# Performance work log

Measured on AMD Instinct MI355X. Metric: run time of the kernel, lower is better.

Reference implementation:

```python
import jax, jax.numpy as jnp
import numpy as np

N_A, N_C, N_L = 50000, 10000, 10000
HID = 128


def _gatv2(x_src, x_dst, src, dst, ea, Wl, bl, Wr, br, We, att, bias, H):
    # GATv2Conv (PyG) bipartite, edge_dim=1, concat=False (mean over heads), eval mode (no dropout)
    C = bias.shape[0]
    n_dst = x_dst.shape[0]
    xl = (x_src @ Wl + bl).reshape(-1, H, C)      # [N_src, H, C]
    xr = (x_dst @ Wr + br).reshape(-1, H, C)      # [N_dst, H, C]
    e = jax.nn.leaky_relu(xl[src] + xr[dst] + (ea @ We).reshape(-1, H, C), 0.2)  # [E,H,C]
    logit = jnp.einsum('ehc,hc->eh', e, att)      # [E,H]
    m = jax.ops.segment_max(logit, dst, num_segments=n_dst)
    m = jax.lax.stop_gradient(jnp.where(jnp.isfinite(m), m, 0.0))
    ex = jnp.exp(logit - m[dst])
    denom = jax.ops.segment_sum(ex, dst, num_segments=n_dst)
    alpha = ex / (denom[dst] + 1e-16)             # segment softmax over incoming edges
    out = jax.ops.segment_sum(alpha[:, :, None] * xl[src], dst, num_segments=n_dst)
    return out.mean(axis=1) + bias                # concat=False -> head mean + bias


def setup_inputs() -> dict:
    key = jax.random.key(0)
    ks = iter(jax.random.split(key, 80))
    def rn(shape, s=1.0):
        return jax.random.normal(next(ks), shape, jnp.float32) * s
    inp = {}
    inp['x_asset'] = rn((N_A, 512))
    inp['x_creator'] = rn((N_C, 2))
    inp['x_licensee'] = rn((N_L, 1))
    # edges: (name, E, src_max, dst_max)
    edges = [('cb', 50000, N_A, N_C), ('lt', 100000, N_A, N_L), ('sim', 200000, N_A, N_A),
             ('fw', 100000, N_A, N_A), ('rcb', 50000, N_C, N_A), ('rlt', 100000, N_L, N_A)]
    for name, E, smax, dmax in edges:
        inp[f'{name}_src'] = jax.random.randint(next(ks), (E,), 0, smax, jnp.int32)
        inp[f'{name}_dst'] = jax.random.randint(next(ks), (E,), 0, dmax, jnp.int32)
        inp[f'ea_{name}'] = rn((E, 1))
    w = 0.05  # param scale
    inp['Wp_a'] = rn((512, HID), w); inp['bp_a'] = rn((HID,), w)
    inp['Wp_c'] = rn((2, HID), w);   inp['bp_c'] = rn((HID,), w)
    inp['Wp_l'] = rn((1, HID), w);   inp['bp_l'] = rn((HID,), w)
    # layer 1: heads=2, stacked over the 6 relations
    H1 = 2
    inp['Wl1'] = rn((6, HID, H1 * HID), w); inp['bl1'] = rn((6, H1 * HID), w)
    inp['Wr1'] = rn((6, HID, H1 * HID), w); inp['br1'] = rn((6, H1 * HID), w)
    inp['We1'] = rn((6, 1, H1 * HID), w)
    inp['att1'] = rn((6, H1, HID), w); inp['bias1'] = rn((6, HID), w)
    # layer 2: heads=1
    inp['Wl2'] = rn((6, HID, HID), w); inp['bl2'] = rn((6, HID), w)
    inp['Wr2'] = rn((6, HID, HID), w); inp['br2'] = rn((6, HID), w)
    inp['We2'] = rn((6, 1, HID), w)
    inp['att2'] = rn((6, 1, HID), w); inp['bias2'] = rn((6, HID), w)
    inp['Wc1'] = rn((HID, HID), w); inp['bc1'] = rn((HID,), w)
    inp['Wc2'] = rn((HID, 3), w);   inp['bc2'] = rn((3,), w)
    inp['query_asset_index'] = 123
    return inp


def reference(x_asset, x_creator, x_licensee, Wp_a, bp_a, Wp_c, bp_c, Wp_l, bp_l,
              Wl1, bl1, Wr1, br1, We1, att1, bias1,
              Wl2, bl2, Wr2, br2, We2, att2, bias2,
              Wc1, bc1, Wc2, bc2,
              ea_cb, ea_lt, ea_sim, ea_fw, ea_rcb, ea_rlt,
              cb_src, cb_dst, lt_src, lt_dst, sim_src, sim_dst,
              fw_src, fw_dst, rcb_src, rcb_dst, rlt_src, rlt_dst,
              query_asset_index):
    x = {'Asset': x_asset @ Wp_a + bp_a,
         'Creator': x_creator @ Wp_c + bp_c,
         'Licensee': x_licensee @ Wp_l + bp_l}
    rels = [('Asset', 'Creator', cb_src, cb_dst, ea_cb),
            ('Asset', 'Licensee', lt_src, lt_dst, ea_lt),
            ('Asset', 'Asset', sim_src, sim_dst, ea_sim),
            ('Asset', 'Asset', fw_src, fw_dst, ea_fw),
            ('Creator', 'Asset', rcb_src, rcb_dst, ea_rcb),
            ('Licensee', 'Asset', rlt_src, rlt_dst, ea_rlt)]

    def hetero_layer(x, Wl, bl, Wr, br, We, att, bias, H):
        out = {k: jnp.zeros((v.shape[0], HID), v.dtype) for k, v in x.items()}
        for i, (st, dt, s, d, ea) in enumerate(rels):  # HeteroConv aggr='sum'
            out[dt] = out[dt] + _gatv2(x[st], x[dt], s, d, ea,
                                       Wl[i], bl[i], Wr[i], br[i], We[i], att[i], bias[i], H)
        return out

    x = hetero_layer(x, Wl1, bl1, Wr1, br1, We1, att1, bias1, 2)
    x = {k: jax.nn.relu(v) for k, v in x.items()}  # eval: dropout is identity
    x = hetero_layer(x, Wl2, bl2, Wr2, br2, We2, att2, bias2, 1)
    x = {k: jax.nn.relu(v) for k, v in x.items()}
    a = x['Asset'][query_asset_index]
    return jax.nn.relu(a @ Wc1 + bc1) @ Wc2 + bc2
```

## Files before the change

kernel.cpp:

```cpp
#include <hip/hip_runtime.h>
#include <math.h>

#define FAMAX 512
#define FCMAX 256
#define FLMAX 256
#define N1MAX 4096
#define N2MAX 512

struct Inputs {
  const float *x_asset, *x_creator, *x_licensee;
  const float *Wp_a,*bp_a,*Wp_c,*bp_c,*Wp_l,*bp_l;
  const float *Wl1,*bl1,*Wr1,*br1,*We1,*att1,*bias1;
  const float *Wl2,*bl2,*Wr2,*br2,*We2,*att2,*bias2;
  const float *Wc1,*bc1,*Wc2,*bc2;
};

struct Edges {
  const int *cb_s,*cb_d;  const float* ea_cb;  int Ecb;
  const int *lt_s,*lt_d;  const float* ea_lt;  int Elt;
  const int *sim_s,*sim_d;const float* ea_sim; int Esim;
  const int *fw_s,*fw_d;  const float* ea_fw;  int Efw;
  const int *rcb_s,*rcb_d;const float* ea_rcb; int Ercb;
  const int *rlt_s,*rlt_d;const float* ea_rlt; int Erlt;
};

struct WSP {
  int* cnt;
  int* flagA; int* flagC; int* flagL;
  int* fa; int* fc; int* fl;
  int* l2rel; int* l2src; float* l2ea;
  int* l1rel; int* l1src; int* l1dslot; float* l1ea;
  float* xr1a;
  float* xr1c;
  float* xr1l;
  float* xl1e;
  float* logit1;
  float* x1a;
  float* x1c;
  float* x1l;
  float* xr2q;
  float* xl2e;
  float* logit2;
};

__device__ __forceinline__ float leaky(float x){ return x > 0.f ? x : 0.2f*x; }

__device__ void proj_node(int type, int node, const Inputs& in, float* h0){
  int t = threadIdx.x;
  if (t < 128) {
    float acc;
    if (type == 0) {
      acc = in.bp_a[t];
      const float* xr = in.x_asset + (long long)node*512;
      for (int k=0;k<512;k++) acc = fmaf(xr[k], in.Wp_a[k*128+t], acc);
    } else if (type == 1) {
      acc = in.bp_c[t] + in.x_creator[node*2]*in.Wp_c[t] + in.x_creator[node*2+1]*in.Wp_c[128+t];
    } else {
      acc = in.bp_l[t] + in.x_licensee[node]*in.Wp_l[t];
    }
    h0[t] = acc;
  }
  __syncthreads();
}

__global__ void k1_scan_l2(Edges eg, const int* qptr, WSP w){
  int q = qptr[0];
  if (blockIdx.x==0 && threadIdx.x==0) w.flagA[q] = 1;
  int total = eg.Esim + eg.Efw + eg.Ercb + eg.Erlt;
  for (int i = blockIdx.x*blockDim.x + threadIdx.x; i < total; i += gridDim.x*blockDim.x){
    int j = i, rel; const int *sp,*dp; const float* ep;
    if (j < eg.Esim){ rel=2; sp=eg.sim_s; dp=eg.sim_d; ep=eg.ea_sim; }
    else { j -= eg.Esim;
      if (j < eg.Efw){ rel=3; sp=eg.fw_s; dp=eg.fw_d; ep=eg.ea_fw; }
      else { j -= eg.Efw;
        if (j < eg.Ercb){ rel=4; sp=eg.rcb_s; dp=eg.rcb_d; ep=eg.ea_rcb; }
        else { j -= eg.Ercb; rel=5; sp=eg.rlt_s; dp=eg.rlt_d; ep=eg.ea_rlt; }
      }
    }
    if (dp[j] == q){
      int src = sp[j];
      int k = atomicAdd(&w.cnt[0], 1);
      if (k < N2MAX){ w.l2rel[k]=rel; w.l2src[k]=src; w.l2ea[k]=ep[j]; }
      if (rel <= 3) w.flagA[src] = 1;
      else if (rel == 4) w.flagC[src] = 1;
      else w.flagL[src] = 1;
    }
  }
}

__global__ void k2_compact(WSP w){
  int i = blockIdx.x*blockDim.x + threadIdx.x;
  if (i < 50000){
    if (w.flagA[i] == 1){ int k = atomicAdd(&w.cnt[1],1);
      if (k < FAMAX){ w.flagA[i]=k+2; w.fa[k]=i; } else w.flagA[i]=0; }
  } else if (i < 60000){ int n=i-50000;
    if (w.flagC[n] == 1){ int k = atomicAdd(&w.cnt[2],1);
      if (k < FCMAX){ w.flagC[n]=k+2; w.fc[k]=n; } else w.flagC[n]=0; }
  } else if (i < 70000){ int n=i-60000;
    if (w.flagL[n] == 1){ int k = atomicAdd(&w.cnt[3],1);
      if (k < FLMAX){ w.flagL[n]=k+2; w.fl[k]=n; } else w.flagL[n]=0; }
  }
}

__global__ void k3_scan_l1(Edges eg, WSP w){
  int total = eg.Ecb+eg.Elt+eg.Esim+eg.Efw+eg.Ercb+eg.Erlt;
  for (int i = blockIdx.x*blockDim.x + threadIdx.x; i < total; i += gridDim.x*blockDim.x){
    int j = i, rel; const int *sp,*dp; const float* ep; const int* flag;
    if (j < eg.Ecb){ rel=0; sp=eg.cb_s; dp=eg.cb_d; ep=eg.ea_cb; flag=w.flagC; }
    else { j -= eg.Ecb;
    if (j < eg.Elt){ rel=1; sp=eg.lt_s; dp=eg.lt_d; ep=eg.ea_lt; flag=w.flagL; }
    else { j -= eg.Elt;
    if (j < eg.Esim){ rel=2; sp=eg.sim_s; dp=eg.sim_d; ep=eg.ea_sim; flag=w.flagA; }
    else { j -= eg.Esim;
    if (j < eg.Efw){ rel=3; sp=eg.fw_s; dp=eg.fw_d; ep=eg.ea_fw; flag=w.flagA; }
    else { j -= eg.Efw;
    if (j < eg.Ercb){ rel=4; sp=eg.rcb_s; dp=eg.rcb_d; ep=eg.ea_rcb; flag=w.flagA; }
    else { j -= eg.Ercb; rel=5; sp=eg.rlt_s; dp=eg.rlt_d; ep=eg.ea_rlt; flag=w.flagA; }}}}}
    int f = flag[dp[j]];
    if (f >= 2){
      int k = atomicAdd(&w.cnt[4], 1);
      if (k < N1MAX){ w.l1rel[k]=rel; w.l1src[k]=sp[j]; w.l1dslot[k]=f-2; w.l1ea[k]=ep[j]; }
    }
  }
}

__global__ void k4_xr1(Inputs in, WSP w){
  __shared__ float h0[128];
  int b = blockIdx.x;
  int na = w.cnt[1] < FAMAX ? w.cnt[1] : FAMAX;
  int nc = w.cnt[2] < FCMAX ? w.cnt[2] : FCMAX;
  int nl = w.cnt[3] < FLMAX ? w.cnt[3] : FLMAX;
  int rel; float* dst;
  if (b < FAMAX*4){
    int slot = b>>2, ridx = b&3;
    if (slot >= na) return;
    rel = 2 + ridx;
    proj_node(0, w.fa[slot], in, h0);
    dst = w.xr1a + ((size_t)slot*4 + ridx)*256;
  } else if (b < FAMAX*4 + FCMAX){
    int slot = b - FAMAX*4;
    if (slot >= nc) return;
    rel = 0;
    proj_node(1, w.fc[slot], in, h0);
    dst = w.xr1c + (size_t)slot*256;
  } else {
    int slot = b - FAMAX*4 - FCMAX;
    if (slot >= nl) return;
    rel = 1;
    proj_node(2, w.fl[slot], in, h0);
    dst = w.xr1l + (size_t)slot*256;
  }
  int j = threadIdx.x;
  float acc = in.br1[rel*256 + j];
  const float* W = in.Wr1 + (size_t)rel*128*256;
  for (int c=0;c<128;c++) acc = fmaf(h0[c], W[c*256 + j], acc);
  dst[j] = acc;
}

__global__ void k5_l1edge(Inputs in, WSP w){
  __shared__ float h0[128];
  __shared__ float red[256];
  int i = blockIdx.x;
  int n = w.cnt[4] < N1MAX ? w.cnt[4] : N1MAX;
  if (i >= n) return;
  int rel = w.l1rel[i], src = w.l1src[i], dslot = w.l1dslot[i];
  float ea = w.l1ea[i];
  int stype = (rel <= 3) ? 0 : (rel == 4 ? 1 : 2);
  proj_node(stype, src, in, h0);
  int j = threadIdx.x;
  float acc = in.bl1[rel*256 + j];
  const float* W = in.Wl1 + (size_t)rel*128*256;
  for (int c=0;c<128;c++) acc = fmaf(h0[c], W[c*256 + j], acc);
  w.xl1e[(size_t)i*256 + j] = acc;
  const float* xr;
  if (rel >= 2) xr = w.xr1a + ((size_t)dslot*4 + (rel-2))*256;
  else if (rel == 0) xr = w.xr1c + (size_t)dslot*256;
  else xr = w.xr1l + (size_t)dslot*256;
  float e = leaky(acc + xr[j] + ea*in.We1[rel*256 + j]);
  int h = j >> 7, c = j & 127;
  red[j] = e * in.att1[(rel*2 + h)*128 + c];
  __syncthreads();
  for (int s=64; s>0; s>>=1){ if (c < s) red[j] += red[j+s]; __syncthreads(); }
  if (c == 0) w.logit1[i*2 + h] = red[j];
}

__global__ void k6_agg(Inputs in, WSP w){
  int b = blockIdx.x;
  int na = w.cnt[1] < FAMAX ? w.cnt[1] : FAMAX;
  int nc = w.cnt[2] < FCMAX ? w.cnt[2] : FCMAX;
  int nl = w.cnt[3] < FLMAX ? w.cnt[3] : FLMAX;
  int type, slot;
  if (b < FAMAX){ slot = b; if (slot >= na) return; type = 0; }
  else if (b < FAMAX+FCMAX){ slot = b-FAMAX; if (slot >= nc) return; type = 1; }
  else { slot = b-FAMAX-FCMAX; if (slot >= nl) return; type = 2; }
  int n1 = w.cnt[4] < N1MAX ? w.cnt[4] : N1MAX;
  int j = threadIdx.x;
  float out = 0.f;
  int r0, r1;
  if (type == 0){ r0=2; r1=5; } else if (type == 1){ r0=0; r1=0; } else { r0=1; r1=1; }
  for (int r=r0; r<=r1; r++){
    out += in.bias1[r*128 + j];
    float m0 = -INFINITY, m1 = -INFINITY;
    for (int i=0;i<n1;i++){
      if (w.l1rel[i]==r && w.l1dslot[i]==slot){
        m0 = fmaxf(m0, w.logit1[i*2]);
        m1 = fmaxf(m1, w.logit1[i*2+1]);
      }
    }
    if (m0 == -INFINITY) continue;
    float d0=0.f, d1=0.f, a0=0.f, a1=0.f;
    for (int i=0;i<n1;i++){
      if (w.l1rel[i]==r && w.l1dslot[i]==slot){
        float e0 = expf(w.logit1[i*2]   - m0);
        float e1 = expf(w.logit1[i*2+1] - m1);
        d0 += e0; d1 += e1;
        a0 = fmaf(e0, w.xl1e[(size_t)i*256 + j], a0);
        a1 = fmaf(e1, w.xl1e[(size_t)i*256 + 128 + j], a1);
      }
    }
    out += 0.5f*(a0/(d0+1e-16f) + a1/(d1+1e-16f));
  }
  float v = fmaxf(out, 0.f);
  if (type == 0) w.x1a[slot*128 + j] = v;
  else if (type == 1) w.x1c[slot*128 + j] = v;
  else w.x1l[slot*128 + j] = v;
}

__global__ void k7_xr2(Inputs in, WSP w, const int* qptr){
  int q = qptr[0];
  int qslot = w.flagA[q] - 2;
  const float* xq = w.x1a + (size_t)qslot*128;
  int j = threadIdx.x;
  for (int ridx=0; ridx<4; ridx++){
    int r = 2 + ridx;
    float acc = in.br2[r*128 + j];
    const float* W = in.Wr2 + (size_t)r*128*128;
    for (int c=0;c<128;c++) acc = fmaf(xq[c], W[c*128 + j], acc);
    w.xr2q[ridx*128 + j] = acc;
  }
}

__global__ void k8_l2edge(Inputs in, WSP w){
  __shared__ float red[128];
  int i = blockIdx.x;
  int n2 = w.cnt[0] < N2MAX ? w.cnt[0] : N2MAX;
  if (i >= n2) return;
  int rel = w.l2rel[i], src = w.l2src[i];
  float ea = w.l2ea[i];
  int f;
  const float* xbase;
  if (rel <= 3){ f = w.flagA[src]; xbase = w.x1a; }
  else if (rel == 4){ f = w.flagC[src]; xbase = w.x1c; }
  else { f = w.flagL[src]; xbase = w.x1l; }
  if (f < 2) return;
  const float* xsrc = xbase + (size_t)(f-2)*128;
  int j = threadIdx.x;
  float acc = in.bl2[rel*128 + j];
  const float* W = in.Wl2 + (size_t)rel*128*128;
  for (int c=0;c<128;c++) acc = fmaf(xsrc[c], W[c*128 + j], acc);
  w.xl2e[(size_t)i*128 + j] = acc;
  float e = leaky(acc + w.xr2q[(rel-2)*128 + j] + ea*in.We2[rel*128 + j]);
  red[j] = e * in.att2[rel*128 + j];
  __syncthreads();
  for (int s=64; s>0; s>>=1){ if (j < s) red[j] += red[j+s]; __syncthreads(); }
  if (j == 0) w.logit2[i] = red[0];
}

__global__ void k9_final(Inputs in, WSP w, float* out){
  __shared__ float x2[128];
  __shared__ float t[128];
  int n2 = w.cnt[0] < N2MAX ? w.cnt[0] : N2MAX;
  int j = threadIdx.x;
  float o = 0.f;
  for (int r=2; r<=5; r++){
    o += in.bias2[r*128 + j];
    float m = -INFINITY;
    for (int i=0;i<n2;i++) if (w.l2rel[i]==r) m = fmaxf(m, w.logit2[i]);
    if (m == -INFINITY) continue;
    float d = 0.f, acc = 0.f;
    for (int i=0;i<n2;i++) if (w.l2rel[i]==r){
      float e = expf(w.logit2[i] - m);
      d += e;
      acc = fmaf(e, w.xl2e[(size_t)i*128 + j], acc);
    }
    o += acc/(d + 1e-16f);
  }
  x2[j] = fmaxf(o, 0.f);
  __syncthreads();
  float acc = in.bc1[j];
  for (int c=0;c<128;c++) acc = fmaf(x2[c], in.Wc1[c*128 + j], acc);
  t[j] = fmaxf(acc, 0.f);
  __syncthreads();
  if (j < 3){
    float r = in.bc2[j];
    for (int c=0;c<128;c++) r = fmaf(t[c], in.Wc2[c*3 + j], r);
    out[j] = r;
  }
}

extern "C" void kernel_launch(void* const* d_in, const int* in_sizes, int n_in,
                              void* d_out, int out_size, void* d_ws, size_t ws_size,
                              hipStream_t stream){
  Inputs in;
  in.x_asset   = (const float*)d_in[0];
  in.x_creator = (const float*)d_in[1];
  in.x_licensee= (const float*)d_in[2];
  Edges eg;
  eg.cb_s =(const int*)d_in[3];  eg.cb_d =(const int*)d_in[4];  eg.ea_cb =(const float*)d_in[5];  eg.Ecb = in_sizes[3];
  eg.lt_s =(const int*)d_in[6];  eg.lt_d =(const int*)d_in[7];  eg.ea_lt =(const float*)d_in[8];  eg.Elt = in_sizes[6];
  eg.sim_s=(const int*)d_in[9];  eg.sim_d=(const int*)d_in[10]; eg.ea_sim=(const float*)d_in[11]; eg.Esim= in_sizes[9];
  eg.fw_s =(const int*)d_in[12]; eg.fw_d =(const int*)d_in[13]; eg.ea_fw =(const float*)d_in[14]; eg.Efw = in_sizes[12];
  eg.rcb_s=(const int*)d_in[15]; eg.rcb_d=(const int*)d_in[16]; eg.ea_rcb=(const float*)d_in[17]; eg.Ercb= in_sizes[15];
  eg.rlt_s=(const int*)d_in[18]; eg.rlt_d=(const int*)d_in[19]; eg.ea_rlt=(const float*)d_in[20]; eg.Erlt= in_sizes[18];
  in.Wp_a=(const float*)d_in[21]; in.bp_a=(const float*)d_in[22];
  in.Wp_c=(const float*)d_in[23]; in.bp_c=(const float*)d_in[24];
  in.Wp_l=(const float*)d_in[25]; in.bp_l=(const float*)d_in[26];
  in.Wl1=(const float*)d_in[27]; in.bl1=(const float*)d_in[28];
  in.Wr1=(const float*)d_in[29]; in.br1=(const float*)d_in[30];
  in.We1=(const float*)d_in[31]; in.att1=(const float*)d_in[32]; in.bias1=(const float*)d_in[33];
  in.Wl2=(const float*)d_in[34]; in.bl2=(const float*)d_in[35];
  in.Wr2=(const float*)d_in[36]; in.br2=(const float*)d_in[37];
  in.We2=(const float*)d_in[38]; in.att2=(const float*)d_in[39]; in.bias2=(const float*)d_in[40];
  in.Wc1=(const float*)d_in[41]; in.bc1=(const float*)d_in[42];
  in.Wc2=(const float*)d_in[43]; in.bc2=(const float*)d_in[44];
  const int* qptr = (const int*)d_in[45];

  char* p = (char*)d_ws;
  auto carve = [&](size_t n)->char*{ char* r = p; p += ((n + 255) & ~(size_t)255); return r; };
  WSP w;
  w.cnt    = (int*)carve(16*4);
  w.flagA  = (int*)carve(50000*4);
  w.flagC  = (int*)carve(10000*4);
  w.flagL  = (int*)carve(10000*4);
  size_t zero_bytes = (size_t)(p - (char*)d_ws);
  w.fa = (int*)carve(FAMAX*4); w.fc = (int*)carve(FCMAX*4); w.fl = (int*)carve(FLMAX*4);
  w.l2rel=(int*)carve(N2MAX*4); w.l2src=(int*)carve(N2MAX*4); w.l2ea=(float*)carve(N2MAX*4);
  w.l1rel=(int*)carve(N1MAX*4); w.l1src=(int*)carve(N1MAX*4); w.l1dslot=(int*)carve(N1MAX*4); w.l1ea=(float*)carve(N1MAX*4);
  w.xr1a=(float*)carve((size_t)FAMAX*4*256*4);
  w.xr1c=(float*)carve((size_t)FCMAX*256*4);
  w.xr1l=(float*)carve((size_t)FLMAX*256*4);
  w.xl1e=(float*)carve((size_t)N1MAX*256*4);
  w.logit1=(float*)carve((size_t)N1MAX*2*4);
  w.x1a=(float*)carve((size_t)FAMAX*128*4);
  w.x1c=(float*)carve((size_t)FCMAX*128*4);
  w.x1l=(float*)carve((size_t)FLMAX*128*4);
  w.xr2q=(float*)carve(4*128*4);
  w.xl2e=(float*)carve((size_t)N2MAX*128*4);
  w.logit2=(float*)carve(N2MAX*4);

  hipMemsetAsync(d_ws, 0, zero_bytes, stream);

  int tE2 = eg.Esim + eg.Efw + eg.Ercb + eg.Erlt;
  k1_scan_l2<<<(tE2+255)/256, 256, 0, stream>>>(eg, qptr, w);
  k2_compact<<<(70000+255)/256, 256, 0, stream>>>(w);
  int tE1 = eg.Ecb + eg.Elt + tE2;
  k3_scan_l1<<<(tE1+255)/256, 256, 0, stream>>>(eg, w);
  k4_xr1<<<FAMAX*4 + FCMAX + FLMAX, 256, 0, stream>>>(in, w);
  k5_l1edge<<<N1MAX, 256, 0, stream>>>(in, w);
  k6_agg<<<FAMAX + FCMAX + FLMAX, 128, 0, stream>>>(in, w);
  k7_xr2<<<1, 128, 0, stream>>>(in, w, qptr);
  k8_l2edge<<<N2MAX, 128, 0, stream>>>(in, w);
  k9_final<<<1, 128, 0, stream>>>(in, w, (float*)d_out);
}
```

Measured before the change: 346.8 us.

## Fuse GNN pipeline into five kernels with atomic claim and shrunk capacity caps

Replaces the separate flag-compaction pass with an atomicCAS-based claim done inside the layer-2 edge scan. The xr projection, edge logits and softmax aggregation are fused into a per-node kernel, and the layer-2 xr/edge/final stages are merged into one single-block kernel. Capacity caps (FAMAX, N1MAX, N2MAX and others) are cut sharply, and new DMAX/N2C limits are added. This removes four launches and several large workspace buffers, but node-side work is serialised per edge with block syncs, and the smaller caps can silently drop neighbours if real degrees exceed them.

After: 359.9 us. 1.04x slower.

```diff
diff --git a/kernel.cpp b/kernel.cpp
--- a/kernel.cpp
+++ b/kernel.cpp
@@ -1,11 +1,13 @@
 #include <hip/hip_runtime.h>
 #include <math.h>
 
-#define FAMAX 512
-#define FCMAX 256
-#define FLMAX 256
-#define N1MAX 4096
-#define N2MAX 512
+#define FAMAX 64
+#define FCMAX 32
+#define FLMAX 32
+#define N1MAX 1024
+#define N2MAX 128
+#define DMAX  64
+#define N2C   64
 
 struct Inputs {
   const float *x_asset, *x_creator, *x_licensee;
@@ -30,20 +32,22 @@
   int* fa; int* fc; int* fl;
   int* l2rel; int* l2src; float* l2ea;
   int* l1rel; int* l1src; int* l1dslot; float* l1ea;
-  float* xr1a;
-  float* xr1c;
-  float* xr1l;
   float* xl1e;
-  float* logit1;
   float* x1a;
   float* x1c;
   float* x1l;
-  float* xr2q;
-  float* xl2e;
-  float* logit2;
 };
 
 __device__ __forceinline__ float leaky(float x){ return x > 0.f ? x : 0.2f*x; }
+
+__device__ __forceinline__ void claim(int* flag, int* cnt, int* list, int node, int cap){
+  int old = atomicCAS(&flag[node], 0, 1);
+  if (old == 0){
+    int k = atomicAdd(cnt, 1);
+    if (k < cap){ list[k] = node; atomicExch(&flag[node], k + 2); }
+    else atomicExch(&flag[node], 0);
+  }
+}
 
 __device__ void proj_node(int type, int node, const Inputs& in, float* h0){
   int t = threadIdx.x;
@@ -65,7 +69,7 @@
 
 __global__ void k1_scan_l2(Edges eg, const int* qptr, WSP w){
   int q = qptr[0];
-  if (blockIdx.x==0 && threadIdx.x==0) w.flagA[q] = 1;
+  if (blockIdx.x==0 && threadIdx.x==0) claim(w.flagA, &w.cnt[1], w.fa, q, FAMAX);
   int total = eg.Esim + eg.Efw + eg.Ercb + eg.Erlt;
   for (int i = blockIdx.x*blockDim.x + threadIdx.x; i < total; i += gridDim.x*blockDim.x){
     int j = i, rel; const int *sp,*dp; const float* ep;
@@ -81,28 +85,14 @@
       int src = sp[j];
       int k = atomicAdd(&w.cnt[0], 1);
       if (k < N2MAX){ w.l2rel[k]=rel; w.l2src[k]=src; w.l2ea[k]=ep[j]; }
-      if (rel <= 3) w.flagA[src] = 1;
-      else if (rel == 4) w.flagC[src] = 1;
-      else w.flagL[src] = 1;
-    }
-  }
-}
-
-__global__ void k2_compact(WSP w){
-  int i = blockIdx.x*blockDim.x + threadIdx.x;
-  if (i < 50000){
-    if (w.flagA[i] == 1){ int k = atomicAdd(&w.cnt[1],1);
-      if (k < FAMAX){ w.flagA[i]=k+2; w.fa[k]=i; } else w.flagA[i]=0; }
-  } else if (i < 60000){ int n=i-50000;
-    if (w.flagC[n] == 1){ int k = atomicAdd(&w.cnt[2],1);
-      if (k < FCMAX){ w.flagC[n]=k+2; w.fc[k]=n; } else w.flagC[n]=0; }
-  } else if (i < 70000){ int n=i-60000;
-    if (w.flagL[n] == 1){ int k = atomicAdd(&w.cnt[3],1);
-      if (k < FLMAX){ w.flagL[n]=k+2; w.fl[k]=n; } else w.flagL[n]=0; }
-  }
-}
-
-__global__ void k3_scan_l1(Edges eg, WSP w){
+      if (rel <= 3) claim(w.flagA, &w.cnt[1], w.fa, src, FAMAX);
+      else if (rel == 4) claim(w.flagC, &w.cnt[2], w.fc, src, FCMAX);
+      else claim(w.flagL, &w.cnt[3], w.fl, src, FLMAX);
+    }
+  }
+}
+
+__global__ void k2_scan_l1(Edges eg, WSP w){
   int total = eg.Ecb+eg.Elt+eg.Esim+eg.Efw+eg.Ercb+eg.Erlt;
   for (int i = blockIdx.x*blockDim.x + threadIdx.x; i < total; i += gridDim.x*blockDim.x){
     int j = i, rel; const int *sp,*dp; const float* ep; const int* flag;
@@ -124,47 +114,12 @@
   }
 }
 
-__global__ void k4_xr1(Inputs in, WSP w){
+__global__ void k3_edgeproj(Inputs in, WSP w){
   __shared__ float h0[128];
-  int b = blockIdx.x;
-  int na = w.cnt[1] < FAMAX ? w.cnt[1] : FAMAX;
-  int nc = w.cnt[2] < FCMAX ? w.cnt[2] : FCMAX;
-  int nl = w.cnt[3] < FLMAX ? w.cnt[3] : FLMAX;
-  int rel; float* dst;
-  if (b < FAMAX*4){
-    int slot = b>>2, ridx = b&3;
-    if (slot >= na) return;
-    rel = 2 + ridx;
-    proj_node(0, w.fa[slot], in, h0);
-    dst = w.xr1a + ((size_t)slot*4 + ridx)*256;
-  } else if (b < FAMAX*4 + FCMAX){
-    int slot = b - FAMAX*4;
-    if (slot >= nc) return;
-    rel = 0;
-    proj_node(1, w.fc[slot], in, h0);
-    dst = w.xr1c + (size_t)slot*256;
-  } else {
-    int slot = b - FAMAX*4 - FCMAX;
-    if (slot >= nl) return;
-    rel = 1;
-    proj_node(2, w.fl[slot], in, h0);
-    dst = w.xr1l + (size_t)slot*256;
-  }
-  int j = threadIdx.x;
-  float acc = in.br1[rel*256 + j];
-  const float* W = in.Wr1 + (size_t)rel*128*256;
-  for (int c=0;c<128;c++) acc = fmaf(h0[c], W[c*256 + j], acc);
-  dst[j] = acc;
-}
-
-__global__ void k5_l1edge(Inputs in, WSP w){
-  __shared__ float h0[128];
-  __shared__ float red[256];
   int i = blockIdx.x;
   int n = w.cnt[4] < N1MAX ? w.cnt[4] : N1MAX;
   if (i >= n) return;
-  int rel = w.l1rel[i], src = w.l1src[i], dslot = w.l1dslot[i];
-  float ea = w.l1ea[i];
+  int rel = w.l1rel[i], src = w.l1src[i];
   int stype = (rel <= 3) ? 0 : (rel == 4 ? 1 : 2);
   proj_node(stype, src, in, h0);
   int j = threadIdx.x;
@@ -172,116 +127,127 @@
   const float* W = in.Wl1 + (size_t)rel*128*256;
   for (int c=0;c<128;c++) acc = fmaf(h0[c], W[c*256 + j], acc);
   w.xl1e[(size_t)i*256 + j] = acc;
-  const float* xr;
-  if (rel >= 2) xr = w.xr1a + ((size_t)dslot*4 + (rel-2))*256;
-  else if (rel == 0) xr = w.xr1c + (size_t)dslot*256;
-  else xr = w.xr1l + (size_t)dslot*256;
-  float e = leaky(acc + xr[j] + ea*in.We1[rel*256 + j]);
-  int h = j >> 7, c = j & 127;
-  red[j] = e * in.att1[(rel*2 + h)*128 + c];
-  __syncthreads();
-  for (int s=64; s>0; s>>=1){ if (c < s) red[j] += red[j+s]; __syncthreads(); }
-  if (c == 0) w.logit1[i*2 + h] = red[j];
-}
-
-__global__ void k6_agg(Inputs in, WSP w){
+}
+
+__global__ void k4_nodeagg(Inputs in, WSP w){
+  __shared__ float h0[128];
+  __shared__ float red[256];
+  __shared__ float lg[DMAX][2];
+  __shared__ int   eid[DMAX];
   int b = blockIdx.x;
   int na = w.cnt[1] < FAMAX ? w.cnt[1] : FAMAX;
   int nc = w.cnt[2] < FCMAX ? w.cnt[2] : FCMAX;
   int nl = w.cnt[3] < FLMAX ? w.cnt[3] : FLMAX;
-  int type, slot;
-  if (b < FAMAX){ slot = b; if (slot >= na) return; type = 0; }
-  else if (b < FAMAX+FCMAX){ slot = b-FAMAX; if (slot >= nc) return; type = 1; }
-  else { slot = b-FAMAX-FCMAX; if (slot >= nl) return; type = 2; }
+  int type, slot, node;
+  if (b < FAMAX){ slot=b; if (slot>=na) return; type=0; node=w.fa[slot]; }
+  else if (b < FAMAX+FCMAX){ slot=b-FAMAX; if (slot>=nc) return; type=1; node=w.fc[slot]; }
+  else { slot=b-FAMAX-FCMAX; if (slot>=nl) return; type=2; node=w.fl[slot]; }
+  proj_node(type, node, in, h0);
   int n1 = w.cnt[4] < N1MAX ? w.cnt[4] : N1MAX;
   int j = threadIdx.x;
+  int h = j >> 7, c = j & 127;
   float out = 0.f;
   int r0, r1;
-  if (type == 0){ r0=2; r1=5; } else if (type == 1){ r0=0; r1=0; } else { r0=1; r1=1; }
+  if (type==0){ r0=2; r1=5; } else if (type==1){ r0=0; r1=0; } else { r0=1; r1=1; }
   for (int r=r0; r<=r1; r++){
-    out += in.bias1[r*128 + j];
-    float m0 = -INFINITY, m1 = -INFINITY;
-    for (int i=0;i<n1;i++){
+    if (j < 128) out += in.bias1[r*128 + j];
+    float xr = in.br1[r*256 + j];
+    const float* W = in.Wr1 + (size_t)r*128*256;
+    for (int cc=0;cc<128;cc++) xr = fmaf(h0[cc], W[cc*256 + j], xr);
+    float we = in.We1[r*256 + j];
+    float at = in.att1[(r*2 + h)*128 + c];
+    int nd = 0;
+    for (int i=0;i<n1 && nd<DMAX;i++){
       if (w.l1rel[i]==r && w.l1dslot[i]==slot){
-        m0 = fmaxf(m0, w.logit1[i*2]);
-        m1 = fmaxf(m1, w.logit1[i*2+1]);
+        float e = leaky(w.xl1e[(size_t)i*256 + j] + xr + w.l1ea[i]*we);
+        red[j] = e * at;
+        __syncthreads();
+        for (int s=64; s>0; s>>=1){ if (c < s) red[j] += red[j+s]; __syncthreads(); }
+        if (j == 0){ lg[nd][0] = red[0]; lg[nd][1] = red[128]; eid[nd] = i; }
+        __syncthreads();
+        nd++;
       }
     }
-    if (m0 == -INFINITY) continue;
-    float d0=0.f, d1=0.f, a0=0.f, a1=0.f;
-    for (int i=0;i<n1;i++){
-      if (w.l1rel[i]==r && w.l1dslot[i]==slot){
-        float e0 = expf(w.logit1[i*2]   - m0);
-        float e1 = expf(w.logit1[i*2+1] - m1);
-        d0 += e0; d1 += e1;
-        a0 = fmaf(e0, w.xl1e[(size_t)i*256 + j], a0);
-        a1 = fmaf(e1, w.xl1e[(size_t)i*256 + 128 + j], a1);
+    if (nd == 0) continue;
+    float m0=-INFINITY, m1=-INFINITY;
+    for (int d=0; d<nd; d++){ m0 = fmaxf(m0, lg[d][0]); m1 = fmaxf(m1, lg[d][1]); }
+    float d0=0.f, d1=0.f;
+    for (int d=0; d<nd; d++){ d0 += expf(lg[d][0]-m0); d1 += expf(lg[d][1]-m1); }
+    if (j < 128){
+      float a0=0.f, a1=0.f;
+      for (int d=0; d<nd; d++){
+        int i = eid[d];
+        a0 = fmaf(expf(lg[d][0]-m0), w.xl1e[(size_t)i*256 + j],       a0);
+        a1 = fmaf(expf(lg[d][1]-m1), w.xl1e[(size_t)i*256 + 128 + j], a1);
       }
-    }
-    out += 0.5f*(a0/(d0+1e-16f) + a1/(d1+1e-16f));
-  }
-  float v = fmaxf(out, 0.f);
-  if (type == 0) w.x1a[slot*128 + j] = v;
-  else if (type == 1) w.x1c[slot*128 + j] = v;
-  else w.x1l[slot*128 + j] = v;
-}
-
-__global__ void k7_xr2(Inputs in, WSP w, const int* qptr){
+      out += 0.5f*(a0/(d0+1e-16f) + a1/(d1+1e-16f));
+    }
+    __syncthreads();
+  }
+  if (j < 128){
+    float v = fmaxf(out, 0.f);
+    if (type==0) w.x1a[slot*128 + j] = v;
+    else if (type==1) w.x1c[slot*128 + j] = v;
+    else w.x1l[slot*128 + j] = v;
+  }
+}
+
+__global__ void k5_final(Inputs in, WSP w, const int* qptr, float* outp){
+  __shared__ float xq[128];
+  __shared__ float xs[128];
+  __shared__ float red[128];
+  __shared__ float xlc[N2C][128];
+  __shared__ float lg[N2C];
+  __shared__ int   srel[N2C];
+  __shared__ float x2[128];
+  __shared__ float t[128];
+  int j = threadIdx.x;
   int q = qptr[0];
-  int qslot = w.flagA[q] - 2;
-  const float* xq = w.x1a + (size_t)qslot*128;
-  int j = threadIdx.x;
+  int qs = w.flagA[q] - 2;
+  xq[j] = w.x1a[(size_t)qs*128 + j];
+  __syncthreads();
+  float xr2r[4];
   for (int ridx=0; ridx<4; ridx++){
     int r = 2 + ridx;
     float acc = in.br2[r*128 + j];
     const float* W = in.Wr2 + (size_t)r*128*128;
     for (int c=0;c<128;c++) acc = fmaf(xq[c], W[c*128 + j], acc);
-    w.xr2q[ridx*128 + j] = acc;
-  }
-}
-
-__global__ void k8_l2edge(Inputs in, WSP w){
-  __shared__ float red[128];
-  int i = blockIdx.x;
+    xr2r[ridx] = acc;
+  }
   int n2 = w.cnt[0] < N2MAX ? w.cnt[0] : N2MAX;
-  if (i >= n2) return;
-  int rel = w.l2rel[i], src = w.l2src[i];
-  float ea = w.l2ea[i];
-  int f;
-  const float* xbase;
-  if (rel <= 3){ f = w.flagA[src]; xbase = w.x1a; }
-  else if (rel == 4){ f = w.flagC[src]; xbase = w.x1c; }
-  else { f = w.flagL[src]; xbase = w.x1l; }
-  if (f < 2) return;
-  const float* xsrc = xbase + (size_t)(f-2)*128;
-  int j = threadIdx.x;
-  float acc = in.bl2[rel*128 + j];
-  const float* W = in.Wl2 + (size_t)rel*128*128;
-  for (int c=0;c<128;c++) acc = fmaf(xsrc[c], W[c*128 + j], acc);
-  w.xl2e[(size_t)i*128 + j] = acc;
-  float e = leaky(acc + w.xr2q[(rel-2)*128 + j] + ea*in.We2[rel*128 + j]);
-  red[j] = e * in.att2[rel*128 + j];
-  __syncthreads();
-  for (int s=64; s>0; s>>=1){ if (j < s) red[j] += red[j+s]; __syncthreads(); }
-  if (j == 0) w.logit2[i] = red[0];
-}
-
-__global__ void k9_final(Inputs in, WSP w, float* out){
-  __shared__ float x2[128];
-  __shared__ float t[128];
-  int n2 = w.cnt[0] < N2MAX ? w.cnt[0] : N2MAX;
-  int j = threadIdx.x;
+  if (n2 > N2C) n2 = N2C;
+  for (int i=0;i<n2;i++){
+    int rel = w.l2rel[i], src = w.l2src[i];
+    float ea = w.l2ea[i];
+    int f; const float* xb;
+    if (rel <= 3){ f = w.flagA[src]; xb = w.x1a; }
+    else if (rel == 4){ f = w.flagC[src]; xb = w.x1c; }
+    else { f = w.flagL[src]; xb = w.x1l; }
+    if (f < 2){ if (j==0) srel[i] = -1; __syncthreads(); continue; }
+    xs[j] = xb[(size_t)(f-2)*128 + j];
+    __syncthreads();
+    float acc = in.bl2[rel*128 + j];
+    const float* W = in.Wl2 + (size_t)rel*128*128;
+    for (int c=0;c<128;c++) acc = fmaf(xs[c], W[c*128 + j], acc);
+    xlc[i][j] = acc;
+    float e = leaky(acc + xr2r[rel-2] + ea*in.We2[rel*128 + j]);
+    red[j] = e * in.att2[rel*128 + j];
+    __syncthreads();
+    for (int s=64; s>0; s>>=1){ if (j < s) red[j] += red[j+s]; __syncthreads(); }
+    if (j == 0){ lg[i] = red[0]; srel[i] = rel; }
+    __syncthreads();
+  }
   float o = 0.f;
   for (int r=2; r<=5; r++){
     o += in.bias2[r*128 + j];
     float m = -INFINITY;
-    for (int i=0;i<n2;i++) if (w.l2rel[i]==r) m = fmaxf(m, w.logit2[i]);
+    for (int i=0;i<n2;i++) if (srel[i]==r) m = fmaxf(m, lg[i]);
     if (m == -INFINITY) continue;
     float d = 0.f, acc = 0.f;
-    for (int i=0;i<n2;i++) if (w.l2rel[i]==r){
-      float e = expf(w.logit2[i] - m);
+    for (int i=0;i<n2;i++) if (srel[i]==r){
+      float e = expf(lg[i] - m);
       d += e;
-      acc = fmaf(e, w.xl2e[(size_t)i*128 + j], acc);
+      acc = fmaf(e, xlc[i][j], acc);
     }
     o += acc/(d + 1e-16f);
   }
@@ -294,7 +260,7 @@
   if (j < 3){
     float r = in.bc2[j];
     for (int c=0;c<128;c++) r = fmaf(t[c], in.Wc2[c*3 + j], r);
-    out[j] = r;
+    outp[j] = r;
   }
 }
 
@@ -336,29 +302,18 @@
   w.fa = (int*)carve(FAMAX*4); w.fc = (int*)carve(FCMAX*4); w.fl = (int*)carve(FLMAX*4);
   w.l2rel=(int*)carve(N2MAX*4); w.l2src=(int*)carve(N2MAX*4); w.l2ea=(float*)carve(N2MAX*4);
   w.l1rel=(int*)carve(N1MAX*4); w.l1src=(int*)carve(N1MAX*4); w.l1dslot=(int*)carve(N1MAX*4); w.l1ea=(float*)carve(N1MAX*4);
-  w.xr1a=(float*)carve((size_t)FAMAX*4*256*4);
-  w.xr1c=(float*)carve((size_t)FCMAX*256*4);
-  w.xr1l=(float*)carve((size_t)FLMAX*256*4);
   w.xl1e=(float*)carve((size_t)N1MAX*256*4);
-  w.logit1=(float*)carve((size_t)N1MAX*2*4);
   w.x1a=(float*)carve((size_t)FAMAX*128*4);
   w.x1c=(float*)carve((size_t)FCMAX*128*4);
   w.x1l=(float*)carve((size_t)FLMAX*128*4);
-  w.xr2q=(float*)carve(4*128*4);
-  w.xl2e=(float*)carve((size_t)N2MAX*128*4);
-  w.logit2=(float*)carve(N2MAX*4);
 
   hipMemsetAsync(d_ws, 0, zero_bytes, stream);
 
   int tE2 = eg.Esim + eg.Efw + eg.Ercb + eg.Erlt;
   k1_scan_l2<<<(tE2+255)/256, 256, 0, stream>>>(eg, qptr, w);
-  k2_compact<<<(70000+255)/256, 256, 0, stream>>>(w);
   int tE1 = eg.Ecb + eg.Elt + tE2;
-  k3_scan_l1<<<(tE1+255)/256, 256, 0, stream>>>(eg, w);
-  k4_xr1<<<FAMAX*4 + FCMAX + FLMAX, 256, 0, stream>>>(in, w);
-  k5_l1edge<<<N1MAX, 256, 0, stream>>>(in, w);
-  k6_agg<<<FAMAX + FCMAX + FLMAX, 128, 0, stream>>>(in, w);
-  k7_xr2<<<1, 128, 0, stream>>>(in, w, qptr);
-  k8_l2edge<<<N2MAX, 128, 0, stream>>>(in, w);
-  k9_final<<<1, 128, 0, stream>>>(in, w, (float*)d_out);
-}
+  k2_scan_l1<<<(tE1+255)/256, 256, 0, stream>>>(eg, w);
+  k3_edgeproj<<<N1MAX, 256, 0, stream>>>(in, w);
+  k4_nodeagg<<<FAMAX + FCMAX + FLMAX, 256, 0, stream>>>(in, w);
+  k5_final<<<1, 128, 0, stream>>>(in, w, qptr, (float*)d_out);
+}
```
